# Kernel tuning notes

Measured on AMD Instinct MI355X. Metric: run time of the kernel, lower is better.

## Reference

```python
import jax, jax.numpy as jnp
import numpy as np

N_NODES = 100000
N_EDGES = 800000
NUM_GRAPHS = 64


def _lin_init(key, fan_in, fan_out):
    k1, k2 = jax.random.split(key)
    s = 1.0 / np.sqrt(fan_in)
    W = jax.random.uniform(k1, (fan_in, fan_out), jnp.float32, -s, s)
    b = jax.random.uniform(k2, (fan_out,), jnp.float32, -s, s)
    return W, b


def setup_inputs() -> dict:
    key = jax.random.key(0)
    ks = jax.random.split(key, 20)
    inp = {
        'x1': jax.random.normal(ks[0], (N_NODES, 384), jnp.float32),
        'x2': jax.random.normal(ks[1], (N_NODES, 32), jnp.float32),
        'pe': jax.random.normal(ks[2], (N_NODES, 64), jnp.float32),
        'edge_index': jax.random.randint(ks[3], (2, N_EDGES), 0, N_NODES, jnp.int32),
        'batch': jnp.sort(jax.random.randint(ks[4], (N_NODES,), 0, NUM_GRAPHS, jnp.int32)),
    }
    # parameters (fan_in, fan_out) per __init__ dims
    inp['Wc'], inp['bc'] = _lin_init(ks[5], 384, 192)     # embed_contraction
    inp['Wmf'], inp['bmf'] = _lin_init(ks[6], 192, 256)   # mpnn_feature
    inp['Wgf'], inp['bgf'] = _lin_init(ks[7], 256, 192)   # gcn_feature
    inp['Wmc'], inp['bmc'] = _lin_init(ks[8], 32, 64)     # mpnn_class
    inp['Wgc'], inp['bgc'] = _lin_init(ks[9], 64, 192)    # gcn_class
    inp['Wa1'], inp['ba1'] = _lin_init(ks[10], 192, 256)  # attention_nn[0]
    inp['Wa2'], inp['ba2'] = _lin_init(ks[11], 256, 192)  # attention_nn[2]
    inp['Wgd'], inp['bgd'] = _lin_init(ks[12], 192, 192)  # gcn_decoder
    inp['Wd1'], inp['bd1'] = _lin_init(ks[13], 192, 192)  # mpnn_decoder1
    inp['Wd2'], inp['bd2'] = _lin_init(ks[14], 192, 192)  # mpnn_decoder2
    inp['Wd3'], inp['bd3'] = _lin_init(ks[15], 192, 384)  # mpnn_decoder3
    return inp


def _mpnn(x, src, dst, W, b):
    # aggr='add': scatter-add gathered source features to targets, then Linear
    agg = jax.ops.segment_sum(x[src], dst, num_segments=N_NODES)
    return agg @ W + b


def _gcn(x, src, dst, W, b):
    # GCNConv with default self-loops and symmetric deg^-1/2 normalization
    h = x @ W
    deg = jax.ops.segment_sum(jnp.ones(src.shape[0], h.dtype), dst, num_segments=N_NODES) + 1.0
    dinv = jax.lax.rsqrt(deg)
    norm = dinv[src] * dinv[dst]
    agg = jax.ops.segment_sum(h[src] * norm[:, None], dst, num_segments=N_NODES)
    agg = agg + h * (dinv * dinv)[:, None]  # self-loop contribution
    return agg + b


def reference(x1, x2, pe, edge_index, batch,
              Wc, bc, Wmf, bmf, Wgf, bgf, Wmc, bmc, Wgc, bgc,
              Wa1, ba1, Wa2, ba2, Wgd, bgd, Wd1, bd1, Wd2, bd2, Wd3, bd3):
    src, dst = edge_index[0], edge_index[1]
    pe3 = jnp.concatenate([pe, pe, pe], axis=-1)  # [N, 192]

    # ---- encoder ----
    x1_res = jax.nn.relu(x1 @ Wc + bc)            # [N, 192]
    h = x1_res + pe3
    h = jax.nn.relu(_mpnn(h, src, dst, Wmf, bmf))  # [N, 256]
    h = jax.nn.relu(_gcn(h, src, dst, Wgf, bgf))   # [N, 192]
    c = jax.nn.relu(_mpnn(x2, src, dst, Wmc, bmc)) # [N, 64]
    c = jax.nn.relu(_gcn(c, src, dst, Wgc, bgc))   # [N, 192]
    z = h + c + x1_res

    # attentional aggregation: gate = attention_nn(z), segment softmax, weighted sum
    gate = jax.nn.relu(z @ Wa1 + ba1) @ Wa2 + ba2   # [N, 192]
    gmax = jax.ops.segment_max(gate, batch, num_segments=NUM_GRAPHS)
    e = jnp.exp(gate - gmax[batch])
    esum = jax.ops.segment_sum(e, batch, num_segments=NUM_GRAPHS)
    alpha = e / esum[batch]
    zg = jax.ops.segment_sum(alpha * z, batch, num_segments=NUM_GRAPHS)  # [B, 192]

    # ---- decoder ----
    z1 = zg[batch]                                  # broadcast graph embedding to nodes
    z1_res = jax.nn.relu(_gcn(z1, src, dst, Wgd, bgd))
    t = z1_res + pe3
    t = jax.nn.relu(_mpnn(t, src, dst, Wd1, bd1))
    t = jax.nn.relu(_mpnn(t, src, dst, Wd2, bd2)) + z1_res
    out = jax.nn.relu(_mpnn(t, src, dst, Wd3, bd3))  # [N, 384]
    return out
```

## Files before the change

### kernel.cpp

```cpp
#include <hip/hip_runtime.h>
#include <math.h>

#define N_NODES 100000
#define N_EDGES 800000
#define NGRAPH  64

typedef __attribute__((ext_vector_type(8))) __bf16 bf16x8;
typedef __attribute__((ext_vector_type(4))) float f32x4;

static __device__ __forceinline__ unsigned flip_f(float x) {
  unsigned u = __float_as_uint(x);
  return u ^ ((u & 0x80000000u) ? 0xFFFFFFFFu : 0x80000000u);
}
static __device__ __forceinline__ float unflip_f(unsigned m) {
  unsigned u = m ^ ((m & 0x80000000u) ? 0x80000000u : 0xFFFFFFFFu);
  return __uint_as_float(u);
}
static __device__ __forceinline__ unsigned short f2bf(float x) {
  unsigned u = __float_as_uint(x);
  u += 0x7fffu + ((u >> 16) & 1u);
  return (unsigned short)(u >> 16);
}
static __device__ __forceinline__ unsigned pk2(float a, float b) {
  return (unsigned)f2bf(a) | ((unsigned)f2bf(b) << 16);
}
static __device__ __forceinline__ float bf2f(unsigned short h) {
  return __uint_as_float((unsigned)h << 16);
}
static __device__ __forceinline__ void unpack8(uint4 w, float* f) {
  f[0] = __uint_as_float(w.x << 16); f[1] = __uint_as_float(w.x & 0xFFFF0000u);
  f[2] = __uint_as_float(w.y << 16); f[3] = __uint_as_float(w.y & 0xFFFF0000u);
  f[4] = __uint_as_float(w.z << 16); f[5] = __uint_as_float(w.z & 0xFFFF0000u);
  f[6] = __uint_as_float(w.w << 16); f[7] = __uint_as_float(w.w & 0xFFFF0000u);
}
static __device__ __forceinline__ uint4 pack8(const float* f) {
  uint4 w;
  w.x = pk2(f[0], f[1]); w.y = pk2(f[2], f[3]);
  w.z = pk2(f[4], f[5]); w.w = pk2(f[6], f[7]);
  return w;
}

struct WJobs {
  const float* src[10];
  int K[10];
  int F[10];
  int eoff[10];
  int bend[10];
};

__global__ void wconv_k(WJobs jb, unsigned short* __restrict__ dst) {
  int b = blockIdx.x;
  int j = 0;
#pragma unroll
  for (int t = 0; t < 10; t++)
    if (b >= jb.bend[t]) j = t + 1;
  int bstart = j ? jb.bend[j - 1] : 0;
  int local = (b - bstart) * 256 + threadIdx.x;
  int K = jb.K[j], F = jb.F[j];
  if (local >= K * F) return;
  int n = local / K;
  int k = local - n * K;
  dst[jb.eoff[j] + local] = f2bf(jb.src[j][(size_t)k * F + n]);
}

__global__ void hist_k(const int* __restrict__ dst, int* __restrict__ cnt) {
  int e = blockIdx.x * 256 + threadIdx.x;
  if (e < N_EDGES) atomicAdd(&cnt[dst[e]], 1);
}

__global__ void dinv_k(const int* __restrict__ cnt, float* __restrict__ dinv) {
  int i = blockIdx.x * 256 + threadIdx.x;
  if (i < N_NODES) dinv[i] = rsqrtf((float)cnt[i] + 1.0f);
}

__global__ void scan_block_k(const int* __restrict__ cnt, int* __restrict__ rs,
                             int* __restrict__ bsum) {
  __shared__ int s[256];
  int t = threadIdx.x, i = blockIdx.x * 256 + t;
  int v = (i < N_NODES) ? cnt[i] : 0;
  s[t] = v; __syncthreads();
  for (int off = 1; off < 256; off <<= 1) {
    int a = (t >= off) ? s[t - off] : 0;
    __syncthreads();
    s[t] += a;
    __syncthreads();
  }
  if (i < N_NODES) rs[i] = s[t] - v;
  if (t == 255) bsum[blockIdx.x] = s[255];
}

__global__ void scan_bsum_k(int* __restrict__ bsum, int nb) {
  __shared__ int s[512];
  int t = threadIdx.x;
  int v = (t < nb) ? bsum[t] : 0;
  s[t] = v; __syncthreads();
  for (int off = 1; off < 512; off <<= 1) {
    int a = (t >= off) ? s[t - off] : 0;
    __syncthreads();
    s[t] += a;
    __syncthreads();
  }
  if (t < nb) bsum[t] = s[t] - v;
}

__global__ void scan_add_k(int* __restrict__ rs, int* __restrict__ cursor,
                           const int* __restrict__ bsum) {
  int i = blockIdx.x * 256 + threadIdx.x;
  if (i < N_NODES) {
    int r = rs[i] + bsum[i >> 8];
    rs[i] = r;
    cursor[i] = r;
  }
}

__global__ void build_k(const int* __restrict__ src, const int* __restrict__ dst,
                        int* __restrict__ cursor, int* __restrict__ srcs) {
  int e = blockIdx.x * 256 + threadIdx.x;
  if (e < N_EDGES) {
    int d = dst[e];
    int p = atomicAdd(&cursor[d], 1);
    srcs[p] = src[e];
  }
}

__global__ void graph_starts_k(const int* __restrict__ batch, int* __restrict__ gstart) {
  int g = threadIdx.x;
  if (g > NGRAPH) return;
  if (g == NGRAPH) { gstart[NGRAPH] = N_NODES; return; }
  int lo = 0, hi = N_NODES;
  while (lo < hi) {
    int mid = (lo + hi) >> 1;
    if (batch[mid] < g) lo = mid + 1; else hi = mid;
  }
  gstart[g] = lo;
}

template <typename AT, int K, int KT, int NT, bool OUT_F32, int OCC>
__global__ __launch_bounds__(256, OCC)
void gemm_t(const AT* __restrict__ A, const unsigned short* __restrict__ Bt,
            const float* __restrict__ bias,
            const unsigned short* __restrict__ add1,
            const unsigned short* __restrict__ add2,
            void* __restrict__ Cv, int M, int F, int relu,
            const float* __restrict__ pe3src, unsigned short* __restrict__ C2) {
  constexpr int BN = 16 * NT;
  constexpr int KTILES = K / KT;
  constexpr int NSTEP = KT / 32;
  constexpr int KC = KT / 8;
  constexpr int STK = KT + 8;
  __shared__ unsigned short Bs[BN * STK];
  const int tid = threadIdx.x;
  const int wave = tid >> 6, lane = tid & 63;
  const int quad = lane >> 4, l16 = lane & 15;
  const int row0 = blockIdx.x * 64;
  const int col0 = blockIdx.y * BN;
  const int arow = row0 + wave * 16 + l16;
  const bool aok = arow < M;

  f32x4 acc[NT];
#pragma unroll
  for (int j = 0; j < NT; j++) acc[j] = (f32x4){0.f, 0.f, 0.f, 0.f};

#pragma unroll
  for (int kt = 0; kt < KTILES; ++kt) {
    if (kt) __syncthreads();

    float4 av[sizeof(AT) == 4 ? 2 * NSTEP : 1];
    uint4 ah[sizeof(AT) == 4 ? 1 : NSTEP];
    if constexpr (sizeof(AT) == 4) {
      const float* ap = (const float*)A + (size_t)arow * K + kt * KT + quad * 8;
#pragma unroll
      for (int s = 0; s < NSTEP; s++) {
        av[2 * s] = aok ? *(const float4*)(ap + s * 32) : make_float4(0.f, 0.f, 0.f, 0.f);
        av[2 * s + 1] = aok ? *(const float4*)(ap + s * 32 + 4) : make_float4(0.f, 0.f, 0.f, 0.f);
      }
    } else {
      const unsigned short* ap = (const unsigned short*)A + (size_t)arow * K + kt * KT + quad * 8;
#pragma unroll
      for (int s = 0; s < NSTEP; s++)
        ah[s] = aok ? *(const uint4*)(ap + s * 32) : make_uint4(0, 0, 0, 0);
    }

#pragma unroll
    for (int idx = tid; idx < BN * KC; idx += 256) {
      int n = idx / KC;
      int c = idx - n * KC;
      uint4 w = *(const uint4*)(Bt + (size_t)(col0 + n) * K + kt * KT + c * 8);
      *(uint4*)&Bs[n * STK + c * 8] = w;
    }
    __syncthreads();

#pragma unroll
    for (int s = 0; s < NSTEP; ++s) {
      bf16x8 afr;
      if constexpr (sizeof(AT) == 4) {
        uint4 t;
        t.x = pk2(av[2 * s].x, av[2 * s].y);
        t.y = pk2(av[2 * s].z, av[2 * s].w);
        t.z = pk2(av[2 * s + 1].x, av[2 * s + 1].y);
        t.w = pk2(av[2 * s + 1].z, av[2 * s + 1].w);
        afr = *(bf16x8*)&t;
      } else {
        afr = *(bf16x8*)&ah[s];
      }
#pragma unroll
      for (int nt = 0; nt < NT; nt++) {
        bf16x8 bfr = *(const bf16x8*)&Bs[(nt * 16 + l16) * STK + s * 32 + quad * 8];
        acc[nt] = __builtin_amdgcn_mfma_f32_16x16x32_bf16(afr, bfr, acc[nt], 0, 0, 0);
      }
    }
  }

  float* Cf = (float*)Cv;
  unsigned short* Ch = (unsigned short*)Cv;
#pragma unroll
  for (int r = 0; r < 4; r++) {
    int row = row0 + wave * 16 + quad * 4 + r;
    if (row >= M) continue;
#pragma unroll
    for (int nt = 0; nt < NT; nt++) {
      int col = col0 + nt * 16 + l16;
      float v = acc[nt][r];
      if (bias) v += bias[col];
      if (relu) v = fmaxf(v, 0.f);
      size_t off = (size_t)row * F + col;
      if (add1) v += bf2f(add1[off]);
      if (add2) v += bf2f(add2[off]);
      if (OUT_F32) Cf[off] = v; else Ch[off] = f2bf(v);
      if (C2) C2[off] = f2bf(v + pe3src[(size_t)row * 64 + (col & 63)]);
    }
  }
}

__global__ __launch_bounds__(256)
void gemm_kernel(const float* __restrict__ A, const float* __restrict__ B,
                 const float* __restrict__ bias, float* __restrict__ C,
                 int M, int K, int F) {
  __shared__ float Asm[16][65];
  __shared__ float Bsm[16][65];
  const int tid = threadIdx.x;
  const int tx = tid & 15, ty = tid >> 4;
  const int row0 = blockIdx.x * 64;
  const int col0 = blockIdx.y * 64;
  float acc[4][4];
#pragma unroll
  for (int i = 0; i < 4; i++)
#pragma unroll
    for (int j = 0; j < 4; j++) acc[i][j] = 0.f;

  for (int k0 = 0; k0 < K; k0 += 16) {
#pragma unroll
    for (int l = 0; l < 4; l++) {
      int idx = tid + l * 256;
      int m = idx >> 4, k = idx & 15;
      int r = row0 + m;
      Asm[k][m] = (r < M) ? A[(size_t)r * K + k0 + k] : 0.f;
    }
#pragma unroll
    for (int l = 0; l < 4; l++) {
      int idx = tid + l * 256;
      int k = idx >> 6, n = idx & 63;
      Bsm[k][n] = B[(size_t)(k0 + k) * F + col0 + n];
    }
    __syncthreads();
#pragma unroll
    for (int k = 0; k < 16; k++) {
      float a[4], b[4];
#pragma unroll
      for (int i = 0; i < 4; i++) a[i] = Asm[k][ty * 4 + i];
#pragma unroll
      for (int j = 0; j < 4; j++) b[j] = Bsm[k][tx * 4 + j];
#pragma unroll
      for (int i = 0; i < 4; i++)
#pragma unroll
        for (int j = 0; j < 4; j++) acc[i][j] += a[i] * b[j];
    }
    __syncthreads();
  }
#pragma unroll
  for (int i = 0; i < 4; i++) {
    int r = row0 + ty * 4 + i;
    if (r >= M) continue;
#pragma unroll
    for (int j = 0; j < 4; j++) {
      int c = col0 + tx * 4 + j;
      float v = acc[i][j];
      if (bias) v += bias[c];
      C[(size_t)r * F + c] = v;
    }
  }
}

template <int F>
__global__ void agg_mpnn_bf(const unsigned short* __restrict__ x, const int* __restrict__ rowstart,
                            const int* __restrict__ cnt, const int* __restrict__ srcs,
                            unsigned short* __restrict__ out) {
  constexpr int F8 = F / 8;
  int t = blockIdx.x * 256 + threadIdx.x;
  if (t >= N_NODES * F8) return;
  int i = t / F8, c = (t - i * F8) * 8;
  float a[8] = {0.f, 0.f, 0.f, 0.f, 0.f, 0.f, 0.f, 0.f};
  int e = rowstart[i], e1 = e + cnt[i];
  for (; e < e1; ++e) {
    int s = srcs[e];
    uint4 w = *(const uint4*)(x + (size_t)s * F + c);
    float f[8]; unpack8(w, f);
#pragma unroll
    for (int j = 0; j < 8; j++) a[j] += f[j];
  }
  *(uint4*)(out + (size_t)i * F + c) = pack8(a);
}

template <int F, bool RELU, bool HAS_BIAS>
__global__ void agg_gcn_bf(const unsigned short* __restrict__ x, const int* __restrict__ rowstart,
                           const int* __restrict__ cnt, const int* __restrict__ srcs,
                           const float* __restrict__ dinv, const float* __restrict__ bias,
                           unsigned short* __restrict__ out) {
  constexpr int F8 = F / 8;
  int t = blockIdx.x * 256 + threadIdx.x;
  if (t >= N_NODES * F8) return;
  int i = t / F8, c = (t - i * F8) * 8;
  float a[8] = {0.f, 0.f, 0.f, 0.f, 0.f, 0.f, 0.f, 0.f};
  int e = rowstart[i], e1 = e + cnt[i];
  for (; e < e1; ++e) {
    int s = srcs[e];
    float w = dinv[s];
    uint4 wv = *(const uint4*)(x + (size_t)s * F + c);
    float f[8]; unpack8(wv, f);
#pragma unroll
    for (int j = 0; j < 8; j++) a[j] += w * f[j];
  }
  float di = dinv[i];
  float sw = di * di;
  uint4 sv = *(const uint4*)(x + (size_t)i * F + c);
  float sf[8]; unpack8(sv, sf);
  float r[8];
#pragma unroll
  for (int j = 0; j < 8; j++) {
    float v = di * a[j] + sw * sf[j];
    if (HAS_BIAS) v += bias[c + j];
    if (RELU) v = fmaxf(v, 0.f);
    r[j] = v;
  }
  *(uint4*)(out + (size_t)i * F + c) = pack8(r);
}

__global__ void agg_x2_k(const float* __restrict__ x, const int* __restrict__ rowstart,
                         const int* __restrict__ cnt, const int* __restrict__ srcs,
                         unsigned short* __restrict__ out) {
  int t = blockIdx.x * 256 + threadIdx.x;
  if (t >= N_NODES * 8) return;
  int i = t >> 3, c = (t & 7) * 4;
  float4 acc = make_float4(0.f, 0.f, 0.f, 0.f);
  int e = rowstart[i], e1 = e + cnt[i];
  for (; e < e1; ++e) {
    int s = srcs[e];
    float4 v = *(const float4*)(x + (size_t)s * 32 + c);
    acc.x += v.x; acc.y += v.y; acc.z += v.z; acc.w += v.w;
  }
  ushort4 o;
  o.x = f2bf(acc.x); o.y = f2bf(acc.y); o.z = f2bf(acc.z); o.w = f2bf(acc.w);
  *(ushort4*)(out + (size_t)i * 32 + c) = o;
}

__global__ void agg_gcn_dec_bf(const float* __restrict__ zgW, const int* __restrict__ rowstart,
                               const int* __restrict__ cnt, const int* __restrict__ srcs,
                               const int* __restrict__ batch, const float* __restrict__ dinv,
                               const float* __restrict__ bias, unsigned short* __restrict__ out,
                               const float* __restrict__ pe, unsigned short* __restrict__ out2) {
  int t = blockIdx.x * 256 + threadIdx.x;
  if (t >= N_NODES * 24) return;
  int i = t / 24, c = (t - i * 24) * 8;
  float a[8] = {0.f, 0.f, 0.f, 0.f, 0.f, 0.f, 0.f, 0.f};
  int e = rowstart[i], e1 = e + cnt[i];
  for (; e < e1; ++e) {
    int s = srcs[e];
    float w = dinv[s];
    const float* v = zgW + (size_t)batch[s] * 192 + c;
#pragma unroll
    for (int j = 0; j < 8; j++) a[j] += w * v[j];
  }
  float di = dinv[i];
  float sw = di * di;
  const float* sv = zgW + (size_t)batch[i] * 192 + c;
  float r[8];
#pragma unroll
  for (int j = 0; j < 8; j++)
    r[j] = fmaxf(di * a[j] + sw * sv[j] + bias[c + j], 0.f);
  *(uint4*)(out + (size_t)i * 192 + c) = pack8(r);
  const float* p = pe + (size_t)i * 64 + (c & 63);
  float r2[8];
#pragma unroll
  for (int j = 0; j < 8; j++) r2[j] = r[j] + p[j];
  *(uint4*)(out2 + (size_t)i * 192 + c) = pack8(r2);
}

__global__ void init_gmax_k(unsigned* __restrict__ gmaxu) {
  int t = blockIdx.x * 256 + threadIdx.x;
  if (t < NGRAPH * 192) gmaxu[t] = 0x007FFFFFu;
}

__global__ void seg_max_k(const float* __restrict__ gate, const int* __restrict__ gstart,
                          unsigned* __restrict__ gmaxu) {
  int g = blockIdx.x, f = threadIdx.x;
  int lo = gstart[g], hi = gstart[g + 1];
  int len = hi - lo;
  if (len <= 0) return;
  int per = (len + gridDim.y - 1) / gridDim.y;
  int a = lo + blockIdx.y * per;
  int b = min(a + per, hi);
  if (a >= b) return;
  float m = -INFINITY;
  for (int i = a; i < b; i++) m = fmaxf(m, gate[(size_t)i * 192 + f]);
  atomicMax(&gmaxu[g * 192 + f], flip_f(m));
}

__global__ void seg_sum_k(const float* __restrict__ gate, const unsigned short* __restrict__ z,
                          const int* __restrict__ gstart, const unsigned* __restrict__ gmaxu,
                          float* __restrict__ esum, float* __restrict__ znum) {
  int g = blockIdx.x, f = threadIdx.x;
  int lo = gstart[g], hi = gstart[g + 1];
  int len = hi - lo;
  if (len <= 0) return;
  int per = (len + gridDim.y - 1) / gridDim.y;
  int a = lo + blockIdx.y * per;
  int b = min(a + per, hi);
  if (a >= b) return;
  float gm = unflip_f(gmaxu[g * 192 + f]);
  float se = 0.f, sz = 0.f;
  for (int i = a; i < b; i++) {
    float e = expf(gate[(size_t)i * 192 + f] - gm);
    se += e;
    sz += e * bf2f(z[(size_t)i * 192 + f]);
  }
  atomicAdd(&esum[g * 192 + f], se);
  atomicAdd(&znum[g * 192 + f], sz);
}

__global__ void zg_fin_k(const float* __restrict__ znum, const float* __restrict__ esum,
                         float* __restrict__ zg) {
  int t = blockIdx.x * 256 + threadIdx.x;
  if (t >= NGRAPH * 192) return;
  float es = esum[t];
  zg[t] = (es > 0.f) ? znum[t] / es : 0.f;
}

extern "C" void kernel_launch(void* const* d_in, const int* in_sizes, int n_in,
                              void* d_out, int out_size, void* d_ws, size_t ws_size,
                              hipStream_t stream) {
  const float* x1 = (const float*)d_in[0];
  const float* x2 = (const float*)d_in[1];
  const float* pe = (const float*)d_in[2];
  const int* ei = (const int*)d_in[3];
  const int* src = ei;
  const int* dst = ei + N_EDGES;
  const int* batch = (const int*)d_in[4];
  const float* Wc  = (const float*)d_in[5];  const float* bc  = (const float*)d_in[6];
  const float* Wmf = (const float*)d_in[7];  const float* bmf = (const float*)d_in[8];
  const float* Wgf = (const float*)d_in[9];  const float* bgf = (const float*)d_in[10];
  const float* Wmc = (const float*)d_in[11]; const float* bmc = (const float*)d_in[12];
  const float* Wgc = (const float*)d_in[13]; const float* bgc = (const float*)d_in[14];
  const float* Wa1 = (const float*)d_in[15]; const float* ba1 = (const float*)d_in[16];
  const float* Wa2 = (const float*)d_in[17]; const float* ba2 = (const float*)d_in[18];
  const float* Wgd = (const float*)d_in[19]; const float* bgd = (const float*)d_in[20];
  const float* Wd1 = (const float*)d_in[21]; const float* bd1 = (const float*)d_in[22];
  const float* Wd2 = (const float*)d_in[23]; const float* bd2 = (const float*)d_in[24];
  const float* Wd3 = (const float*)d_in[25]; const float* bd3 = (const float*)d_in[26];
  float* out = (float*)d_out;

  char* base = (char*)d_ws;
  size_t woff = 0;
  auto walloc = [&](size_t bytes) -> void* {
    void* p = base + woff;
    woff = (woff + bytes + 255) & ~(size_t)255;
    return p;
  };
  unsigned short* P0h = (unsigned short*)walloc((size_t)N_NODES * 192 * 2);
  unsigned short* P1h = (unsigned short*)walloc((size_t)N_NODES * 256 * 2);
  unsigned short* P2h = (unsigned short*)walloc((size_t)N_NODES * 192 * 2);
  unsigned short* P5a = (unsigned short*)walloc((size_t)N_NODES * 32 * 2);
  unsigned short* P5b = (unsigned short*)walloc((size_t)N_NODES * 64 * 2);
  unsigned short* P5c = (unsigned short*)walloc((size_t)N_NODES * 64 * 2);
  float* Pg   = (float*)walloc((size_t)N_NODES * 192 * 4);
  float* dinv = (float*)walloc((size_t)N_NODES * 4);
  unsigned short* Wt = (unsigned short*)walloc((size_t)432128 * 2);
  unsigned* gmaxu = (unsigned*)walloc((size_t)NGRAPH * 192 * 4);
  float* esum = (float*)walloc((size_t)NGRAPH * 192 * 4);
  float* znum = (float*)walloc((size_t)NGRAPH * 192 * 4);
  float* zg   = (float*)walloc((size_t)NGRAPH * 192 * 4);
  float* zgW  = (float*)walloc((size_t)NGRAPH * 192 * 4);
  int* cnt      = (int*)walloc((size_t)N_NODES * 4);
  int* rowstart = (int*)walloc((size_t)N_NODES * 4);
  int* cursor   = (int*)walloc((size_t)N_NODES * 4);
  int* srcs     = (int*)walloc((size_t)N_EDGES * 4);
  int* bsum     = (int*)walloc(512 * 4);
  int* gstart   = (int*)walloc(80 * 4);

  unsigned short* P3h = (unsigned short*)d_out;
  unsigned short* P4h = (unsigned short*)((float*)d_out + (size_t)N_NODES * 192);

  const unsigned short* WtWc  = Wt + 0;
  const unsigned short* WtWmf = Wt + 73728;
  const unsigned short* WtWgf = Wt + 122880;
  const unsigned short* WtWmc = Wt + 172032;
  const unsigned short* WtWgc = Wt + 174080;
  const unsigned short* WtWa1 = Wt + 186368;
  const unsigned short* WtWa2 = Wt + 235520;
  const unsigned short* WtWd1 = Wt + 284672;
  const unsigned short* WtWd2 = Wt + 321536;
  const unsigned short* WtWd3 = Wt + 358400;

  const int TB = 256;
  hipMemsetAsync(cnt, 0, N_NODES * sizeof(int), stream);
  hipMemsetAsync(esum, 0, 2 * NGRAPH * 192 * sizeof(float), stream);

  WJobs jb;
  jb.src[0] = Wc;  jb.K[0] = 384; jb.F[0] = 192; jb.eoff[0] = 0;      jb.bend[0] = 288;
  jb.src[1] = Wmf; jb.K[1] = 192; jb.F[1] = 256; jb.eoff[1] = 73728;  jb.bend[1] = 480;
  jb.src[2] = Wgf; jb.K[2] = 256; jb.F[2] = 192; jb.eoff[2] = 122880; jb.bend[2] = 672;
  jb.src[3] = Wmc; jb.K[3] = 32;  jb.F[3] = 64;  jb.eoff[3] = 172032; jb.bend[3] = 680;
  jb.src[4] = Wgc; jb.K[4] = 64;  jb.F[4] = 192; jb.eoff[4] = 174080; jb.bend[4] = 728;
  jb.src[5] = Wa1; jb.K[5] = 192; jb.F[5] = 256; jb.eoff[5] = 186368; jb.bend[5] = 920;
  jb.src[6] = Wa2; jb.K[6] = 256; jb.F[6] = 192; jb.eoff[6] = 235520; jb.bend[6] = 1112;
  jb.src[7] = Wd1; jb.K[7] = 192; jb.F[7] = 192; jb.eoff[7] = 284672; jb.bend[7] = 1256;
  jb.src[8] = Wd2; jb.K[8] = 192; jb.F[8] = 192; jb.eoff[8] = 321536; jb.bend[8] = 1400;
  jb.src[9] = Wd3; jb.K[9] = 192; jb.F[9] = 384; jb.eoff[9] = 358400; jb.bend[9] = 1688;
  wconv_k<<<1688, 256, 0, stream>>>(jb, Wt);

  hist_k<<<(N_EDGES + TB - 1) / TB, TB, 0, stream>>>(dst, cnt);
  dinv_k<<<(N_NODES + TB - 1) / TB, TB, 0, stream>>>(cnt, dinv);
  int nb = (N_NODES + 255) / 256;
  scan_block_k<<<nb, 256, 0, stream>>>(cnt, rowstart, bsum);
  scan_bsum_k<<<1, 512, 0, stream>>>(bsum, nb);
  scan_add_k<<<nb, 256, 0, stream>>>(rowstart, cursor, bsum);
  build_k<<<(N_EDGES + TB - 1) / TB, TB, 0, stream>>>(src, dst, cursor, srcs);
  graph_starts_k<<<1, 128, 0, stream>>>(batch, gstart);

  const int mb64 = (N_NODES + 63) / 64;
  const int ew24 = (N_NODES * 24 + TB - 1) / TB;
  const int ew8 = (N_NODES * 8 + TB - 1) / TB;

  gemm_t<float, 384, 96, 12, false, 4><<<mb64, 256, 0, stream>>>(x1, WtWc, bc, nullptr, nullptr, P0h, N_NODES, 192, 1, pe, P1h);
  agg_mpnn_bf<192><<<ew24, TB, 0, stream>>>(P1h, rowstart, cnt, srcs, P2h);
  gemm_t<unsigned short, 192, 96, 8, false, 6><<<dim3(mb64, 2), 256, 0, stream>>>(P2h, WtWmf, bmf, nullptr, nullptr, P1h, N_NODES, 256, 1, nullptr, nullptr);
  gemm_t<unsigned short, 256, 128, 6, false, 6><<<dim3(mb64, 2), 256, 0, stream>>>(P1h, WtWgf, nullptr, nullptr, nullptr, P3h, N_NODES, 192, 0, nullptr, nullptr);
  agg_gcn_bf<192, true, true><<<ew24, TB, 0, stream>>>(P3h, rowstart, cnt, srcs, dinv, bgf, P4h);
  agg_x2_k<<<ew8, TB, 0, stream>>>(x2, rowstart, cnt, srcs, P5a);
  gemm_t<unsigned short, 32, 32, 4, false, 6><<<mb64, 256, 0, stream>>>(P5a, WtWmc, bmc, nullptr, nullptr, P5b, N_NODES, 64, 1, nullptr, nullptr);
  agg_gcn_bf<64, false, false><<<ew8, TB, 0, stream>>>(P5b, rowstart, cnt, srcs, dinv, nullptr, P5c);
  gemm_t<unsigned short, 64, 64, 6, false, 6><<<dim3(mb64, 2), 256, 0, stream>>>(P5c, WtWgc, bgc, P4h, P0h, P0h, N_NODES, 192, 1, nullptr, nullptr);

  gemm_t<unsigned short, 192, 96, 8, false, 6><<<dim3(mb64, 2), 256, 0, stream>>>(P0h, WtWa1, ba1, nullptr, nullptr, P1h, N_NODES, 256, 1, nullptr, nullptr);
  gemm_t<unsigned short, 256, 128, 6, true, 6><<<dim3(mb64, 2), 256, 0, stream>>>(P1h, WtWa2, ba2, nullptr, nullptr, Pg, N_NODES, 192, 0, nullptr, nullptr);
  init_gmax_k<<<(NGRAPH * 192 + TB - 1) / TB, TB, 0, stream>>>(gmaxu);
  dim3 sg(NGRAPH, 16);
  seg_max_k<<<sg, 192, 0, stream>>>(Pg, gstart, gmaxu);
  seg_sum_k<<<sg, 192, 0, stream>>>(Pg, P0h, gstart, gmaxu, esum, znum);
  zg_fin_k<<<(NGRAPH * 192 + TB - 1) / TB, TB, 0, stream>>>(znum, esum, zg);
  gemm_kernel<<<dim3(1, 3), 256, 0, stream>>>(zg, Wgd, nullptr, zgW, NGRAPH, 192, 192);

  agg_gcn_dec_bf<<<ew24, TB, 0, stream>>>(zgW, rowstart, cnt, srcs, batch, dinv, bgd, P4h, pe, P2h);
  agg_mpnn_bf<192><<<ew24, TB, 0, stream>>>(P2h, rowstart, cnt, srcs, P3h);
  gemm_t<unsigned short, 192, 96, 6, false, 6><<<dim3(mb64, 2), 256, 0, stream>>>(P3h, WtWd1, bd1, nullptr, nullptr, P1h, N_NODES, 192, 1, nullptr, nullptr);
  agg_mpnn_bf<192><<<ew24, TB, 0, stream>>>(P1h, rowstart, cnt, srcs, P2h);
  gemm_t<unsigned short, 192, 96, 6, false, 6><<<dim3(mb64, 2), 256, 0, stream>>>(P2h, WtWd2, bd2, P4h, nullptr, P3h, N_NODES, 192, 1, nullptr, nullptr);
  agg_mpnn_bf<192><<<ew24, TB, 0, stream>>>(P3h, rowstart, cnt, srcs, P2h);
  gemm_t<unsigned short, 192, 96, 8, true, 6><<<dim3(mb64, 3), 256, 0, stream>>>(P2h, WtWd3, bd3, nullptr, nullptr, out, N_NODES, 384, 1, nullptr, nullptr);
  (void)in_sizes; (void)n_in; (void)out_size; (void)ws_size;
}
```

Before: 1.426 ms.

## Make GEMMs persistent with resident weight tile and double-buffered A loads

Replaces the one-strip-per-block GEMM with a persistent kernel: each block loads its full-K weight slice into shared memory once, then walks row strips in a grid-stride loop. For bf16 inputs, the next strip's A fragments are prefetched into registers while the current strip is computed and stored. This is meant to remove repeated weight loads into shared memory and per-k-tile barriers, and to hide global load latency. In exchange it uses larger shared memory per block, more registers, and lower occupancy. Grid sizes and occupancy bounds are retuned per call.

```diff
diff --git a/kernel.cpp b/kernel.cpp
--- a/kernel.cpp
+++ b/kernel.cpp
@@ -135,73 +135,75 @@
   gstart[g] = lo;
 }
 
-template <typename AT, int K, int KT, int NT, bool OUT_F32, int OCC>
+template <typename AT, int K, int NT, int OCC, bool OUT_F32>
 __global__ __launch_bounds__(256, OCC)
-void gemm_t(const AT* __restrict__ A, const unsigned short* __restrict__ Bt,
+void gemm_p(const AT* __restrict__ A, const unsigned short* __restrict__ Bt,
             const float* __restrict__ bias,
             const unsigned short* __restrict__ add1,
             const unsigned short* __restrict__ add2,
             void* __restrict__ Cv, int M, int F, int relu,
             const float* __restrict__ pe3src, unsigned short* __restrict__ C2) {
   constexpr int BN = 16 * NT;
-  constexpr int KTILES = K / KT;
-  constexpr int NSTEP = KT / 32;
-  constexpr int KC = KT / 8;
-  constexpr int STK = KT + 8;
+  constexpr int NFRAG = K / 32;
+  constexpr int STK = K + 8;
+  constexpr bool F32A = (sizeof(AT) == 4);
   __shared__ unsigned short Bs[BN * STK];
   const int tid = threadIdx.x;
   const int wave = tid >> 6, lane = tid & 63;
   const int quad = lane >> 4, l16 = lane & 15;
-  const int row0 = blockIdx.x * 64;
   const int col0 = blockIdx.y * BN;
-  const int arow = row0 + wave * 16 + l16;
-  const bool aok = arow < M;
-
-  f32x4 acc[NT];
-#pragma unroll
-  for (int j = 0; j < NT; j++) acc[j] = (f32x4){0.f, 0.f, 0.f, 0.f};
-
-#pragma unroll
-  for (int kt = 0; kt < KTILES; ++kt) {
-    if (kt) __syncthreads();
-
-    float4 av[sizeof(AT) == 4 ? 2 * NSTEP : 1];
-    uint4 ah[sizeof(AT) == 4 ? 1 : NSTEP];
-    if constexpr (sizeof(AT) == 4) {
-      const float* ap = (const float*)A + (size_t)arow * K + kt * KT + quad * 8;
-#pragma unroll
-      for (int s = 0; s < NSTEP; s++) {
-        av[2 * s] = aok ? *(const float4*)(ap + s * 32) : make_float4(0.f, 0.f, 0.f, 0.f);
-        av[2 * s + 1] = aok ? *(const float4*)(ap + s * 32 + 4) : make_float4(0.f, 0.f, 0.f, 0.f);
+
+  for (int idx = tid; idx < BN * (K / 8); idx += 256) {
+    int n = idx / (K / 8);
+    int c = idx - n * (K / 8);
+    *(uint4*)&Bs[n * STK + c * 8] = *(const uint4*)(Bt + (size_t)(col0 + n) * K + c * 8);
+  }
+  __syncthreads();
+
+  const int nstrips = (M + 63) >> 6;
+
+  struct ABuf {
+    float4 v[F32A ? 2 * NFRAG : 1];
+    uint4 h[F32A ? 1 : NFRAG];
+  };
+
+  auto LOAD = [&](ABuf& b, int strip) {
+    int row = strip * 64 + wave * 16 + l16;
+    bool ok = row < M;
+    if constexpr (F32A) {
+      const float* ap = (const float*)A + (size_t)row * K + quad * 8;
+#pragma unroll
+      for (int s = 0; s < NFRAG; s++) {
+        b.v[2 * s] = ok ? *(const float4*)(ap + s * 32) : make_float4(0.f, 0.f, 0.f, 0.f);
+        b.v[2 * s + 1] = ok ? *(const float4*)(ap + s * 32 + 4) : make_float4(0.f, 0.f, 0.f, 0.f);
       }
     } else {
-      const unsigned short* ap = (const unsigned short*)A + (size_t)arow * K + kt * KT + quad * 8;
-#pragma unroll
-      for (int s = 0; s < NSTEP; s++)
-        ah[s] = aok ? *(const uint4*)(ap + s * 32) : make_uint4(0, 0, 0, 0);
-    }
-
-#pragma unroll
-    for (int idx = tid; idx < BN * KC; idx += 256) {
-      int n = idx / KC;
-      int c = idx - n * KC;
-      uint4 w = *(const uint4*)(Bt + (size_t)(col0 + n) * K + kt * KT + c * 8);
-      *(uint4*)&Bs[n * STK + c * 8] = w;
-    }
-    __syncthreads();
-
-#pragma unroll
-    for (int s = 0; s < NSTEP; ++s) {
+      const unsigned short* ap = (const unsigned short*)A + (size_t)row * K + quad * 8;
+#pragma unroll
+      for (int s = 0; s < NFRAG; s++)
+        b.h[s] = ok ? *(const uint4*)(ap + s * 32) : make_uint4(0, 0, 0, 0);
+    }
+  };
+
+  float* Cf = (float*)Cv;
+  unsigned short* Ch = (unsigned short*)Cv;
+
+  auto CSTORE = [&](ABuf& b, int strip) {
+    f32x4 acc[NT];
+#pragma unroll
+    for (int j = 0; j < NT; j++) acc[j] = (f32x4){0.f, 0.f, 0.f, 0.f};
+#pragma unroll
+    for (int s = 0; s < NFRAG; s++) {
       bf16x8 afr;
-      if constexpr (sizeof(AT) == 4) {
+      if constexpr (F32A) {
         uint4 t;
-        t.x = pk2(av[2 * s].x, av[2 * s].y);
-        t.y = pk2(av[2 * s].z, av[2 * s].w);
-        t.z = pk2(av[2 * s + 1].x, av[2 * s + 1].y);
-        t.w = pk2(av[2 * s + 1].z, av[2 * s + 1].w);
+        t.x = pk2(b.v[2 * s].x, b.v[2 * s].y);
+        t.y = pk2(b.v[2 * s].z, b.v[2 * s].w);
+        t.z = pk2(b.v[2 * s + 1].x, b.v[2 * s + 1].y);
+        t.w = pk2(b.v[2 * s + 1].z, b.v[2 * s + 1].w);
         afr = *(bf16x8*)&t;
       } else {
-        afr = *(bf16x8*)&ah[s];
+        afr = *(bf16x8*)&b.h[s];
       }
 #pragma unroll
       for (int nt = 0; nt < NT; nt++) {
@@ -209,25 +211,47 @@
         acc[nt] = __builtin_amdgcn_mfma_f32_16x16x32_bf16(afr, bfr, acc[nt], 0, 0, 0);
       }
     }
-  }
-
-  float* Cf = (float*)Cv;
-  unsigned short* Ch = (unsigned short*)Cv;
-#pragma unroll
-  for (int r = 0; r < 4; r++) {
-    int row = row0 + wave * 16 + quad * 4 + r;
-    if (row >= M) continue;
-#pragma unroll
-    for (int nt = 0; nt < NT; nt++) {
-      int col = col0 + nt * 16 + l16;
-      float v = acc[nt][r];
-      if (bias) v += bias[col];
-      if (relu) v = fmaxf(v, 0.f);
-      size_t off = (size_t)row * F + col;
-      if (add1) v += bf2f(add1[off]);
-      if (add2) v += bf2f(add2[off]);
-      if (OUT_F32) Cf[off] = v; else Ch[off] = f2bf(v);
-      if (C2) C2[off] = f2bf(v + pe3src[(size_t)row * 64 + (col & 63)]);
+    int row0 = strip * 64;
+#pragma unroll
+    for (int r = 0; r < 4; r++) {
+      int row = row0 + wave * 16 + quad * 4 + r;
+      if (row >= M) continue;
+#pragma unroll
+      for (int nt = 0; nt < NT; nt++) {
+        int col = col0 + nt * 16 + l16;
+        float v = acc[nt][r];
+        if (bias) v += bias[col];
+        if (relu) v = fmaxf(v, 0.f);
+        size_t off = (size_t)row * F + col;
+        if (add1) v += bf2f(add1[off]);
+        if (add2) v += bf2f(add2[off]);
+        if (OUT_F32) Cf[off] = v; else Ch[off] = f2bf(v);
+        if (C2) C2[off] = f2bf(v + pe3src[(size_t)row * 64 + (col & 63)]);
+      }
+    }
+  };
+
+  if constexpr (F32A) {
+    ABuf bufA;
+    for (int s = blockIdx.x; s < nstrips; s += gridDim.x) {
+      LOAD(bufA, s);
+      CSTORE(bufA, s);
+    }
+  } else {
+    ABuf bufA, bufB;
+    int s = blockIdx.x;
+    LOAD(bufA, s);
+    while (true) {
+      int sn = s + gridDim.x;
+      if (sn >= nstrips) { CSTORE(bufA, s); break; }
+      LOAD(bufB, sn);
+      CSTORE(bufA, s);
+      s = sn;
+      sn = s + gridDim.x;
+      if (sn >= nstrips) { CSTORE(bufB, s); break; }
+      LOAD(bufA, sn);
+      CSTORE(bufB, s);
+      s = sn;
     }
   }
 }
@@ -536,22 +560,21 @@
   build_k<<<(N_EDGES + TB - 1) / TB, TB, 0, stream>>>(src, dst, cursor, srcs);
   graph_starts_k<<<1, 128, 0, stream>>>(batch, gstart);
 
-  const int mb64 = (N_NODES + 63) / 64;
   const int ew24 = (N_NODES * 24 + TB - 1) / TB;
   const int ew8 = (N_NODES * 8 + TB - 1) / TB;
 
-  gemm_t<float, 384, 96, 12, false, 4><<<mb64, 256, 0, stream>>>(x1, WtWc, bc, nullptr, nullptr, P0h, N_NODES, 192, 1, pe, P1h);
+  gemm_p<float, 384, 6, 2, false><<<dim3(256, 2), 256, 0, stream>>>(x1, WtWc, bc, nullptr, nullptr, P0h, N_NODES, 192, 1, pe, P1h);
   agg_mpnn_bf<192><<<ew24, TB, 0, stream>>>(P1h, rowstart, cnt, srcs, P2h);
-  gemm_t<unsigned short, 192, 96, 8, false, 6><<<dim3(mb64, 2), 256, 0, stream>>>(P2h, WtWmf, bmf, nullptr, nullptr, P1h, N_NODES, 256, 1, nullptr, nullptr);
-  gemm_t<unsigned short, 256, 128, 6, false, 6><<<dim3(mb64, 2), 256, 0, stream>>>(P1h, WtWgf, nullptr, nullptr, nullptr, P3h, N_NODES, 192, 0, nullptr, nullptr);
+  gemm_p<unsigned short, 192, 8, 3, false><<<dim3(384, 2), 256, 0, stream>>>(P2h, WtWmf, bmf, nullptr, nullptr, P1h, N_NODES, 256, 1, nullptr, nullptr);
+  gemm_p<unsigned short, 256, 6, 3, false><<<dim3(384, 2), 256, 0, stream>>>(P1h, WtWgf, nullptr, nullptr, nullptr, P3h, N_NODES, 192, 0, nullptr, nullptr);
   agg_gcn_bf<192, true, true><<<ew24, TB, 0, stream>>>(P3h, rowstart, cnt, srcs, dinv, bgf, P4h);
   agg_x2_k<<<ew8, TB, 0, stream>>>(x2, rowstart, cnt, srcs, P5a);
-  gemm_t<unsigned short, 32, 32, 4, false, 6><<<mb64, 256, 0, stream>>>(P5a, WtWmc, bmc, nullptr, nullptr, P5b, N_NODES, 64, 1, nullptr, nullptr);
+  gemm_p<unsigned short, 32, 4, 6, false><<<dim3(1563, 1), 256, 0, stream>>>(P5a, WtWmc, bmc, nullptr, nullptr, P5b, N_NODES, 64, 1, nullptr, nullptr);
   agg_gcn_bf<64, false, false><<<ew8, TB, 0, stream>>>(P5b, rowstart, cnt, srcs, dinv, nullptr, P5c);
-  gemm_t<unsigned short, 64, 64, 6, false, 6><<<dim3(mb64, 2), 256, 0, stream>>>(P5c, WtWgc, bgc, P4h, P0h, P0h, N_NODES, 192, 1, nullptr, nullptr);
-
-  gemm_t<unsigned short, 192, 96, 8, false, 6><<<dim3(mb64, 2), 256, 0, stream>>>(P0h, WtWa1, ba1, nullptr, nullptr, P1h, N_NODES, 256, 1, nullptr, nullptr);
-  gemm_t<unsigned short, 256, 128, 6, true, 6><<<dim3(mb64, 2), 256, 0, stream>>>(P1h, WtWa2, ba2, nullptr, nullptr, Pg, N_NODES, 192, 0, nullptr, nullptr);
+  gemm_p<unsigned short, 64, 12, 4, false><<<dim3(1024, 1), 256, 0, stream>>>(P5c, WtWgc, bgc, P4h, P0h, P0h, N_NODES, 192, 1, nullptr, nullptr);
+
+  gemm_p<unsigned short, 192, 8, 3, false><<<dim3(384, 2), 256, 0, stream>>>(P0h, WtWa1, ba1, nullptr, nullptr, P1h, N_NODES, 256, 1, nullptr, nullptr);
+  gemm_p<unsigned short, 256, 6, 3, true><<<dim3(384, 2), 256, 0, stream>>>(P1h, WtWa2, ba2, nullptr, nullptr, Pg, N_NODES, 192, 0, nullptr, nullptr);
   init_gmax_k<<<(NGRAPH * 192 + TB - 1) / TB, TB, 0, stream>>>(gmaxu);
   dim3 sg(NGRAPH, 16);
   seg_max_k<<<sg, 192, 0, stream>>>(Pg, gstart, gmaxu);
@@ -561,10 +584,10 @@
 
   agg_gcn_dec_bf<<<ew24, TB, 0, stream>>>(zgW, rowstart, cnt, srcs, batch, dinv, bgd, P4h, pe, P2h);
   agg_mpnn_bf<192><<<ew24, TB, 0, stream>>>(P2h, rowstart, cnt, srcs, P3h);
-  gemm_t<unsigned short, 192, 96, 6, false, 6><<<dim3(mb64, 2), 256, 0, stream>>>(P3h, WtWd1, bd1, nullptr, nullptr, P1h, N_NODES, 192, 1, nullptr, nullptr);
+  gemm_p<unsigned short, 192, 6, 4, false><<<dim3(512, 2), 256, 0, stream>>>(P3h, WtWd1, bd1, nullptr, nullptr, P1h, N_NODES, 192, 1, nullptr, nullptr);
   agg_mpnn_bf<192><<<ew24, TB, 0, stream>>>(P1h, rowstart, cnt, srcs, P2h);
-  gemm_t<unsigned short, 192, 96, 6, false, 6><<<dim3(mb64, 2), 256, 0, stream>>>(P2h, WtWd2, bd2, P4h, nullptr, P3h, N_NODES, 192, 1, nullptr, nullptr);
+  gemm_p<unsigned short, 192, 6, 4, false><<<dim3(512, 2), 256, 0, stream>>>(P2h, WtWd2, bd2, P4h, nullptr, P3h, N_NODES, 192, 1, nullptr, nullptr);
   agg_mpnn_bf<192><<<ew24, TB, 0, stream>>>(P3h, rowstart, cnt, srcs, P2h);
-  gemm_t<unsigned short, 192, 96, 8, true, 6><<<dim3(mb64, 3), 256, 0, stream>>>(P2h, WtWd3, bd3, nullptr, nullptr, out, N_NODES, 384, 1, nullptr, nullptr);
+  gemm_p<unsigned short, 192, 8, 3, true><<<dim3(256, 3), 256, 0, stream>>>(P2h, WtWd3, bd3, nullptr, nullptr, out, N_NODES, 384, 1, nullptr, nullptr);
   (void)in_sizes; (void)n_in; (void)out_size; (void)ws_size;
 }
```

Result: slower. 1.865 ms (+30.7%).
